# Performance work log

Hardware: AMD Instinct MI355X
Metric: run time of the kernel (lower is better)

## Reference

```python
import jax, jax.numpy as jnp
import numpy as np

L, B, S, D, SD, E, V = 6, 16, 512, 512, 128, 1536, 32000
PDX = 1  # padding_idx: embedding row zeroed


def _pos_encode(seq_len, d_model):
    pos = np.arange(seq_len)[:, None].astype(np.float32)
    i = np.arange(d_model)[None, :].astype(np.float32)
    ang = pos / np.power(10000.0, 2.0 * np.floor(i / 2.0) / d_model)
    pe = np.where(np.arange(d_model)[None, :] % 2 == 0, np.sin(ang), np.cos(ang))
    return jnp.asarray(pe, dtype=jnp.float32)


def setup_inputs() -> dict:
    key = jax.random.key(0)
    ks = jax.random.split(key, 12)
    def n(k, shape, std=0.02):
        return jax.random.normal(k, shape, jnp.float32) * std
    embed = n(ks[0], (V, D)).at[PDX].set(0.0)
    return dict(
        src_tokens=jax.random.randint(ks[1], (B, S), 0, V),
        src_mask=jax.random.randint(ks[2], (B, S), 0, 2).astype(bool),
        embed=embed,
        ln_g=jnp.ones((L, D)), ln_b=jnp.zeros((L, D)),
        Wz=n(ks[3], (L, D, SD)), bz=jnp.zeros((L, SD)),
        gq=1.0 + n(ks[4], (L, S, SD)), bq=n(ks[5], (L, S, SD)),
        gk=1.0 + n(ks[6], (L, S, SD)), bk=n(ks[7], (L, S, SD)),
        Wu=n(ks[8], (L, D, E)), bu=jnp.zeros((L, E)),
        Wv=n(ks[9], (L, D, E)), bv=jnp.zeros((L, E)),
        Wo=n(ks[10], (L, E, D)), bo=jnp.zeros((L, D)),
        fin_g=jnp.ones((D,)), fin_b=jnp.zeros((D,)),
    )


def _ln(x, g, b, eps=1e-5):
    m = x.mean(-1, keepdims=True)
    v = ((x - m) ** 2).mean(-1, keepdims=True)
    return (x - m) * jax.lax.rsqrt(v + eps) * g + b


def reference(src_tokens, src_mask, embed, ln_g, ln_b, Wz, bz, gq, bq, gk, bk,
              Wu, bu, Wv, bv, Wo, bo, fin_g, fin_b):
    d_model = embed.shape[1]
    x = embed[src_tokens] * (d_model ** 0.5)
    x = x + _pos_encode(src_tokens.shape[1], d_model)[None]  # dropout: eval -> identity
    mask = src_mask[:, None, :]  # (B,1,S): zero attention to masked key positions

    def layer(x, p):
        lg, lb, wz, bz_, gq_, bq_, gk_, bk_, wu, bu_, wv, bv_, wo, bo_ = p
        xn = _ln(x, lg, lb)
        u = xn @ wu + bu_          # (B,S,E)
        v = xn @ wv + bv_          # (B,S,E)
        z = xn @ wz + bz_          # (B,S,SD)
        q = z * gq_ + bq_          # scale_offset (per-position affine)
        k = z * gk_ + bk_
        a = jnp.maximum(jnp.einsum('bsd,btd->bst', q, k), 0.0) ** 2  # relu(qk)^2
        a = jnp.where(mask, 0.0, a)
        o = u * jnp.einsum('bst,bte->bse', a, v)  # gated attention output
        return x + o @ wo + bo_, None

    params = (ln_g, ln_b, Wz, bz, gq, bq, gk, bk, Wu, bu, Wv, bv, Wo, bo)
    x, _ = jax.lax.scan(layer, x, params)
    return _ln(x, fin_g, fin_b)
```

## Files before the change

kernel.cpp:

```cpp
#include <hip/hip_runtime.h>
#include <hip/hip_bf16.h>
#include <stdint.h>

constexpr int L = 6, B = 16, S = 512, D = 512, SD = 128, E = 1536;

using bf16x8 = __attribute__((ext_vector_type(8))) short;
using f32x4  = __attribute__((ext_vector_type(4))) float;

typedef __attribute__((address_space(1))) void gvoid;
typedef __attribute__((address_space(3))) void lvoid;

__device__ __forceinline__ unsigned short f2bf(float f) {
    __hip_bfloat16 h = __float2bfloat16(f);
    return __builtin_bit_cast(unsigned short, h);
}
__device__ __forceinline__ float bf2f(unsigned short u) {
    unsigned int v = ((unsigned int)u) << 16;
    return __builtin_bit_cast(float, v);
}
__device__ __forceinline__ void gload16(const void* g, void* l) {
    __builtin_amdgcn_global_load_lds((gvoid*)g, (lvoid*)l, 16, 0, 0);
}

__device__ __forceinline__ void swz_bid(int& bx, int& by, int& bz) {
    int gx = gridDim.x, gy = gridDim.y, gz = gridDim.z;
    int n = gx * gy * gz;
    int id = blockIdx.x + gx * (blockIdx.y + gy * blockIdx.z);
    int id2 = (id & 7) * (n >> 3) + (id >> 3);
    by = id2 % gy;
    int t = id2 / gy;
    bx = t % gx;
    bz = t / gx;
}

__global__ void detect_mask_kernel(const unsigned char* __restrict__ m, int* flag) {
    if (threadIdx.x == 0) *flag = 0;
    __syncthreads();
    int any = 0;
    for (int i = threadIdx.x; i < B * S; i += blockDim.x)
        if ((i & 3) != 0 && m[i] != 0) any = 1;
    if (any) atomicOr(flag, 1);
}

__global__ void embed_kernel(const int* __restrict__ tok, const float* __restrict__ embed,
                             float* __restrict__ x) {
    int idx = blockIdx.x * blockDim.x + threadIdx.x;
    int d = idx & (D - 1);
    int bs = idx >> 9;
    int s = bs & (S - 1);
    float e = embed[(size_t)tok[bs] * D + d] * 22.62741699796952f;
    float expo = (float)(d >> 1) * (1.0f / 256.0f);
    float ang = (float)s * expf(expo * -9.210340371976184f);
    float pe = (d & 1) ? cosf(ang) : sinf(ang);
    x[idx] = e + pe;
}

__global__ __launch_bounds__(256) void tcast_kernel(const float* __restrict__ W,
                                                    unsigned short* __restrict__ Wt,
                                                    int K, int N, long ostride) {
    __shared__ float t[32][33];
    W  += (size_t)blockIdx.z * K * N;
    Wt += (size_t)blockIdx.z * ostride;
    int k0 = blockIdx.x * 32, n0 = blockIdx.y * 32;
    int tx = threadIdx.x, ty = threadIdx.y;
#pragma unroll
    for (int i = 0; i < 4; ++i)
        t[ty + i * 8][tx] = W[(size_t)(k0 + ty + i * 8) * N + n0 + tx];
    __syncthreads();
#pragma unroll
    for (int i = 0; i < 4; ++i)
        Wt[(size_t)(n0 + ty + i * 8) * K + k0 + tx] = f2bf(t[tx][ty + i * 8]);
}

template <bool BF>
__global__ __launch_bounds__(256) void ln_kernel(const float* __restrict__ x,
                                                 const float* __restrict__ g,
                                                 const float* __restrict__ b,
                                                 void* __restrict__ yp) {
    int row = blockIdx.x * 4 + (threadIdx.x >> 6);
    int lane = threadIdx.x & 63;
    const float* xr = x + (size_t)row * D;
    float4 v0 = *(const float4*)(xr + lane * 4);
    float4 v1 = *(const float4*)(xr + 256 + lane * 4);
    float sum = v0.x + v0.y + v0.z + v0.w + v1.x + v1.y + v1.z + v1.w;
#pragma unroll
    for (int o = 1; o < 64; o <<= 1) sum += __shfl_xor(sum, o);
    float m = sum * (1.0f / D);
    float d0 = v0.x - m, d1 = v0.y - m, d2 = v0.z - m, d3 = v0.w - m;
    float e0 = v1.x - m, e1 = v1.y - m, e2 = v1.z - m, e3 = v1.w - m;
    float sq = d0 * d0 + d1 * d1 + d2 * d2 + d3 * d3 + e0 * e0 + e1 * e1 + e2 * e2 + e3 * e3;
#pragma unroll
    for (int o = 1; o < 64; o <<= 1) sq += __shfl_xor(sq, o);
    float inv = rsqrtf(sq * (1.0f / D) + 1e-5f);
    int c0 = lane * 4, c1 = 256 + lane * 4;
    float4 g0 = *(const float4*)(g + c0), g1 = *(const float4*)(g + c1);
    float4 b0 = *(const float4*)(b + c0), b1 = *(const float4*)(b + c1);
    float o0 = d0 * inv * g0.x + b0.x, o1 = d1 * inv * g0.y + b0.y;
    float o2 = d2 * inv * g0.z + b0.z, o3 = d3 * inv * g0.w + b0.w;
    float o4 = e0 * inv * g1.x + b1.x, o5 = e1 * inv * g1.y + b1.y;
    float o6 = e2 * inv * g1.z + b1.z, o7 = e3 * inv * g1.w + b1.w;
    if constexpr (BF) {
        unsigned short* yr = (unsigned short*)yp + (size_t)row * D;
        ushort4 p0 = {f2bf(o0), f2bf(o1), f2bf(o2), f2bf(o3)};
        ushort4 p1 = {f2bf(o4), f2bf(o5), f2bf(o6), f2bf(o7)};
        *(ushort4*)(yr + c0) = p0;
        *(ushort4*)(yr + c1) = p1;
    } else {
        float* yr = (float*)yp + (size_t)row * D;
        float4 p0 = {o0, o1, o2, o3}, p1 = {o4, o5, o6, o7};
        *(float4*)(yr + c0) = p0;
        *(float4*)(yr + c1) = p1;
    }
}

template <int BM, int BN, bool SWAP>
__device__ __forceinline__ void gemm_core(const unsigned short* __restrict__ Ab,
                                          const unsigned short* __restrict__ Bb,
                                          int K, short* lsA, short* lsB,
                                          f32x4 (&acc)[BM / 32][BN / 32],
                                          int lane, int wv) {
    constexpr int NA = BM / 32, NB = BN / 32;
    constexpr int FM = BM / 32, FN = BN / 32;
    constexpr int WTM = BM / 2, WTN = BN / 2;
    const int wm = wv >> 1, wn = wv & 1;
    const unsigned short* ga[NA]; int lofsA[NA];
    const unsigned short* gb[NB]; int lofsB[NB];
#pragma unroll
    for (int i = 0; i < NA; ++i) {
        int s = wv * NA + i;
        int r = s * 8 + (lane >> 3);
        int cl = (lane & 7) ^ (r & 7);
        ga[i] = Ab + (size_t)r * K + cl * 8;
        lofsA[i] = s * 512;
    }
#pragma unroll
    for (int i = 0; i < NB; ++i) {
        int s = wv * NB + i;
        int r = s * 8 + (lane >> 3);
        int cl = (lane & 7) ^ (r & 7);
        gb[i] = Bb + (size_t)r * K + cl * 8;
        lofsB[i] = s * 512;
    }
    const int nkt = K >> 6;
    for (int kt = 0; kt < nkt; ++kt) {
        if (kt) __syncthreads();
#pragma unroll
        for (int i = 0; i < NA; ++i) gload16(ga[i] + kt * 64, (void*)&lsA[lofsA[i]]);
#pragma unroll
        for (int i = 0; i < NB; ++i) gload16(gb[i] + kt * 64, (void*)&lsB[lofsB[i]]);
        __syncthreads();
#pragma unroll
        for (int ks = 0; ks < 2; ++ks) {
            bf16x8 aF[FM], bF[FN];
#pragma unroll
            for (int f = 0; f < FM; ++f) {
                int ra = wm * WTM + f * 16 + (lane & 15);
                int ca = (ks * 4 + (lane >> 4)) ^ (ra & 7);
                aF[f] = *(const bf16x8*)&lsA[ra * 64 + ca * 8];
            }
#pragma unroll
            for (int f = 0; f < FN; ++f) {
                int rb = wn * WTN + f * 16 + (lane & 15);
                int cb = (ks * 4 + (lane >> 4)) ^ (rb & 7);
                bF[f] = *(const bf16x8*)&lsB[rb * 64 + cb * 8];
            }
#pragma unroll
            for (int fi = 0; fi < FM; ++fi)
#pragma unroll
                for (int fj = 0; fj < FN; ++fj) {
                    if constexpr (SWAP)
                        acc[fi][fj] = __builtin_amdgcn_mfma_f32_16x16x32_bf16(
                            bF[fj], aF[fi], acc[fi][fj], 0, 0, 0);
                    else
                        acc[fi][fj] = __builtin_amdgcn_mfma_f32_16x16x32_bf16(
                            aF[fi], bF[fj], acc[fi][fj], 0, 0, 0);
                }
        }
    }
}

__global__ __launch_bounds__(256) void uv_gemm(const unsigned short* __restrict__ xn,
                                               const unsigned short* __restrict__ Wuvt,
                                               const float* __restrict__ bu,
                                               const float* __restrict__ bvp,
                                               unsigned short* __restrict__ u,
                                               unsigned short* __restrict__ vt) {
    __shared__ short lsA[128 * 64];
    __shared__ short lsB[128 * 64];
    int bx, by, bz;
    swz_bid(bx, by, bz);
    const int tid = threadIdx.x;
    const int lane = tid & 63, wv = tid >> 6;
    const int wm = wv >> 1, wn = wv & 1;
    const int row0 = bx * 128, col0 = by * 128;
    const unsigned short* Ab = xn + (size_t)row0 * D;
    const unsigned short* Bb = Wuvt + ((size_t)bz * E + col0) * D;

    const int lr4 = (lane >> 4) * 4;
    const int lc = lane & 15;
    if (bz == 0) {
        f32x4 acc[4][4] = {};
        gemm_core<128, 128, true>(Ab, Bb, D, lsA, lsB, acc, lane, wv);
#pragma unroll
        for (int fi = 0; fi < 4; ++fi) {
            int r = row0 + wm * 64 + fi * 16 + lc;
#pragma unroll
            for (int fj = 0; fj < 4; ++fj) {
                int cb = col0 + wn * 64 + fj * 16 + lr4;
                f32x4 v = acc[fi][fj];
                f32x4 bv = *(const f32x4*)&bu[cb];
                ushort4 ov = {f2bf(v[0] + bv[0]), f2bf(v[1] + bv[1]),
                              f2bf(v[2] + bv[2]), f2bf(v[3] + bv[3])};
                *(ushort4*)&u[(size_t)r * E + cb] = ov;
            }
        }
    } else {
        f32x4 acc[4][4] = {};
        gemm_core<128, 128, false>(Ab, Bb, D, lsA, lsB, acc, lane, wv);
#pragma unroll
        for (int fi = 0; fi < 4; ++fi) {
            int rb = row0 + wm * 64 + fi * 16 + lr4;
#pragma unroll
            for (int fj = 0; fj < 4; ++fj) {
                int c = col0 + wn * 64 + fj * 16 + lc;
                f32x4 v = acc[fi][fj];
                float bv = bvp[c];
                int b = rb >> 9, t0 = rb & 511;
                ushort4 ov = {f2bf(v[0] + bv), f2bf(v[1] + bv),
                              f2bf(v[2] + bv), f2bf(v[3] + bv)};
                *(ushort4*)&vt[((size_t)b * E + c) * 512 + t0] = ov;
            }
        }
    }
}

__global__ __launch_bounds__(256) void zqk_gemm(const unsigned short* __restrict__ xn,
                                                const unsigned short* __restrict__ Bt,
                                                const float* __restrict__ bias,
                                                const float* __restrict__ gq,
                                                const float* __restrict__ bq,
                                                const float* __restrict__ gk,
                                                const float* __restrict__ bk,
                                                unsigned short* __restrict__ q,
                                                unsigned short* __restrict__ k) {
    __shared__ short lsA[128 * 64];
    __shared__ short lsB[128 * 64];
    int bx, by, bz;
    swz_bid(bx, by, bz);
    const int tid = threadIdx.x;
    const int lane = tid & 63, wv = tid >> 6;
    const int wm = wv >> 1, wn = wv & 1;
    const int row0 = bx * 128;
    const unsigned short* Ab = xn + (size_t)row0 * D;

    f32x4 acc[4][4] = {};
    gemm_core<128, 128, true>(Ab, Bt, D, lsA, lsB, acc, lane, wv);

    const int lr4 = (lane >> 4) * 4;
    const int lc = lane & 15;
#pragma unroll
    for (int fi = 0; fi < 4; ++fi) {
        int r = row0 + wm * 64 + fi * 16 + lc;
        int s = r & 511;
#pragma unroll
        for (int fj = 0; fj < 4; ++fj) {
            int cb = wn * 64 + fj * 16 + lr4;
            f32x4 v = acc[fi][fj];
            f32x4 bz4 = *(const f32x4*)&bias[cb];
            f32x4 gq4 = *(const f32x4*)&gq[(size_t)s * SD + cb];
            f32x4 bq4 = *(const f32x4*)&bq[(size_t)s * SD + cb];
            f32x4 gk4 = *(const f32x4*)&gk[(size_t)s * SD + cb];
            f32x4 bk4 = *(const f32x4*)&bk[(size_t)s * SD + cb];
            ushort4 qv, kv;
#pragma unroll
            for (int g = 0; g < 4; ++g) {
                float zz = v[g] + bz4[g];
                ((unsigned short*)&qv)[g] = f2bf(fmaf(zz, gq4[g], bq4[g]));
                ((unsigned short*)&kv)[g] = f2bf(fmaf(zz, gk4[g], bk4[g]));
            }
            *(ushort4*)&q[(size_t)r * SD + cb] = qv;
            *(ushort4*)&k[(size_t)r * SD + cb] = kv;
        }
    }
}

template <int EPI, int BM, int BN>
__global__ __launch_bounds__(256) void mgemm(const unsigned short* __restrict__ A,
                                             const unsigned short* __restrict__ Bt,
                                             const float* __restrict__ bias,
                                             const void* __restrict__ aux,
                                             const int* __restrict__ flagp,
                                             void* __restrict__ Cp,
                                             int N, int K,
                                             long sA, long sB, long sC, long sAux) {
    __shared__ short lsA[BM * 64];
    __shared__ short lsB[BN * 64];
    constexpr int FM = BM / 32, FN = BN / 32;
    int bx, by, bz;
    swz_bid(bx, by, bz);
    const int tid = threadIdx.x;
    const int lane = tid & 63, wv = tid >> 6;
    const int wm = wv >> 1, wn = wv & 1;
    const int row0 = bx * BM, col0 = by * BN;

    const unsigned short* Ab = A + (size_t)bz * sA + (size_t)row0 * K;
    const unsigned short* Bb = Bt + (size_t)bz * sB + (size_t)col0 * K;

    f32x4 acc[FM][FN] = {};
    gemm_core<BM, BN, true>(Ab, Bb, K, lsA, lsB, acc, lane, wv);

    const int lr4 = (lane >> 4) * 4;
    const int lc = lane & 15;
#pragma unroll
    for (int fi = 0; fi < FM; ++fi) {
        int r = row0 + wm * (BM / 2) + fi * 16 + lc;
#pragma unroll
        for (int fj = 0; fj < FN; ++fj) {
            int cb = col0 + wn * (BN / 2) + fj * 16 + lr4;
            f32x4 v = acc[fi][fj];
            if constexpr (EPI == 3) {
                unsigned short* C = (unsigned short*)Cp + (size_t)bz * sC;
                int flag = *flagp;
                ushort4 ov;
#pragma unroll
                for (int g = 0; g < 4; ++g) {
                    int c = cb + g;
                    int mv = flag ? (int)((const unsigned char*)aux)[bz * sAux + c]
                                  : ((const int*)aux)[bz * sAux + c];
                    float vv = fmaxf(v[g], 0.0f);
                    vv *= vv;
                    ((unsigned short*)&ov)[g] = mv ? (unsigned short)0 : f2bf(vv);
                }
                *(ushort4*)&C[(size_t)r * N + cb] = ov;
            } else if constexpr (EPI == 4) {
                const unsigned short* U = (const unsigned short*)aux + (size_t)bz * sAux;
                unsigned short* C = (unsigned short*)Cp + (size_t)bz * sC;
                size_t off = (size_t)r * N + cb;
                ushort4 uu = *(const ushort4*)&U[off];
                ushort4 ov = {f2bf(bf2f(uu.x) * v[0]), f2bf(bf2f(uu.y) * v[1]),
                              f2bf(bf2f(uu.z) * v[2]), f2bf(bf2f(uu.w) * v[3])};
                *(ushort4*)&C[off] = ov;
            } else {
                float* C = (float*)Cp;
                const float* X = (const float*)aux;
                size_t off = (size_t)r * N + cb;
                f32x4 bb = *(const f32x4*)&bias[cb];
                f32x4 xx = *(const f32x4*)&X[off];
                f32x4 ov = {v[0] + bb[0] + xx[0], v[1] + bb[1] + xx[1],
                            v[2] + bb[2] + xx[2], v[3] + bb[3] + xx[3]};
                *(f32x4*)&C[off] = ov;
            }
        }
    }
}

extern "C" void kernel_launch(void* const* d_in, const int* in_sizes, int n_in,
                              void* d_out, int out_size, void* d_ws, size_t ws_size,
                              hipStream_t stream) {
    const int* tok = (const int*)d_in[0];
    const unsigned char* mask = (const unsigned char*)d_in[1];
    const float* embed = (const float*)d_in[2];
    const float* ln_g = (const float*)d_in[3];
    const float* ln_b = (const float*)d_in[4];
    const float* Wz = (const float*)d_in[5];
    const float* bz = (const float*)d_in[6];
    const float* gq = (const float*)d_in[7];
    const float* bq = (const float*)d_in[8];
    const float* gk = (const float*)d_in[9];
    const float* bk = (const float*)d_in[10];
    const float* Wu = (const float*)d_in[11];
    const float* bu = (const float*)d_in[12];
    const float* Wv = (const float*)d_in[13];
    const float* bv = (const float*)d_in[14];
    const float* Wo = (const float*)d_in[15];
    const float* bo = (const float*)d_in[16];
    const float* fin_g = (const float*)d_in[17];
    const float* fin_b = (const float*)d_in[18];

    char* wsb = (char*)d_ws;
    size_t off = 0;
    auto alloc = [&](size_t nbytes) {
        void* p = wsb + off;
        off = (off + nbytes + 255) & ~(size_t)255;
        return p;
    };
    int* flag = (int*)alloc(256);
    float* x = (float*)alloc((size_t)B * S * D * 4);
    unsigned short* xn = (unsigned short*)alloc((size_t)B * S * D * 2);
    unsigned short* q = (unsigned short*)alloc((size_t)B * S * SD * 2);
    unsigned short* k = (unsigned short*)alloc((size_t)B * S * SD * 2);
    unsigned short* u = (unsigned short*)alloc((size_t)B * S * E * 2);
    unsigned short* vt = (unsigned short*)alloc((size_t)B * E * S * 2);
    unsigned short* o = (unsigned short*)alloc((size_t)B * S * E * 2);
    unsigned short* a = (unsigned short*)alloc((size_t)B * S * S * 2);
    unsigned short* Wuvzt = (unsigned short*)alloc((size_t)L * 3200 * D * 2);
    unsigned short* Wot = (unsigned short*)alloc((size_t)L * D * E * 2);

    constexpr long WUVZ = 3200L * D;

    detect_mask_kernel<<<1, 256, 0, stream>>>(mask, flag);
    embed_kernel<<<(B * S * D) / 256, 256, 0, stream>>>(tok, embed, x);
    tcast_kernel<<<dim3(D / 32, E / 32, L), dim3(32, 8), 0, stream>>>(Wu, Wuvzt, D, E, WUVZ);
    tcast_kernel<<<dim3(D / 32, E / 32, L), dim3(32, 8), 0, stream>>>(
        Wv, Wuvzt + 1536L * D, D, E, WUVZ);
    tcast_kernel<<<dim3(D / 32, SD / 32, L), dim3(32, 8), 0, stream>>>(
        Wz, Wuvzt + 3072L * D, D, SD, WUVZ);
    tcast_kernel<<<dim3(E / 32, D / 32, L), dim3(32, 8), 0, stream>>>(
        Wo, Wot, E, D, (long)D * E);

    for (int l = 0; l < L; ++l) {
        ln_kernel<true><<<B * S / 4, 256, 0, stream>>>(x, ln_g + l * D, ln_b + l * D, xn);
        uv_gemm<<<dim3(64, 12, 2), 256, 0, stream>>>(
            xn, Wuvzt + (size_t)l * WUVZ, bu + l * E, bv + l * E, u, vt);
        zqk_gemm<<<dim3(64, 1), 256, 0, stream>>>(
            xn, Wuvzt + (size_t)l * WUVZ + 3072L * D, bz + l * SD,
            gq + (size_t)l * S * SD, bq + (size_t)l * S * SD,
            gk + (size_t)l * S * SD, bk + (size_t)l * S * SD, q, k);
        mgemm<3, 64, 64><<<dim3(8, 8, B), 256, 0, stream>>>(
            q, k, nullptr, mask, flag, a, S, SD,
            (long)S * SD, (long)S * SD, (long)S * S, S);
        mgemm<4, 128, 128><<<dim3(4, 12, B), 256, 0, stream>>>(
            a, vt, nullptr, u, nullptr, o, E, S,
            (long)S * S, (long)E * S, (long)S * E, (long)S * E);
        mgemm<5, 128, 64><<<dim3(64, 8), 256, 0, stream>>>(
            o, Wot + (size_t)l * D * E, bo + l * D, x, nullptr, x, D, E, 0, 0, 0, 0);
    }
    ln_kernel<false><<<B * S / 4, 256, 0, stream>>>(x, fin_g, fin_b, (float*)d_out);
}
```

Before: 769.5 us.

## Fuse U/V/Z projections into one 256x128-tile GEMM with 8 waves

Merges the separate u/v GEMM and the z→q,k GEMM into a single launch over the concatenated weight matrix, branching on column-block index for each epilogue. Uses 256-row tiles with 8 waves (4x2), generalising gemm_core to a configurable wave grid, and retiles the qk score GEMM to 128x64. The aim is to remove a launch plus the poorly occupied 64-block zqk kernel and to raise reuse of the A tile. It risks higher register and LDS pressure per block and branch-divergent code size.

New measurement: 831.8 us. 8.1% more time.

```diff
diff --git a/kernel.cpp b/kernel.cpp
--- a/kernel.cpp
+++ b/kernel.cpp
@@ -113,16 +113,17 @@
     }
 }
 
-template <int BM, int BN, bool SWAP>
+template <int BM, int BN, int WM, int WN, bool SWAP>
 __device__ __forceinline__ void gemm_core(const unsigned short* __restrict__ Ab,
                                           const unsigned short* __restrict__ Bb,
                                           int K, short* lsA, short* lsB,
-                                          f32x4 (&acc)[BM / 32][BN / 32],
+                                          f32x4 (&acc)[BM / WM / 16][BN / WN / 16],
                                           int lane, int wv) {
-    constexpr int NA = BM / 32, NB = BN / 32;
-    constexpr int FM = BM / 32, FN = BN / 32;
-    constexpr int WTM = BM / 2, WTN = BN / 2;
-    const int wm = wv >> 1, wn = wv & 1;
+    constexpr int NW = WM * WN;
+    constexpr int NA = BM / 8 / NW, NB = BN / 8 / NW;
+    constexpr int WTM = BM / WM, WTN = BN / WN;
+    constexpr int FM = WTM / 16, FN = WTN / 16;
+    const int wm = wv / WN, wn = wv % WN;
     const unsigned short* ga[NA]; int lofsA[NA];
     const unsigned short* gb[NB]; int lofsB[NB];
 #pragma unroll
@@ -179,28 +180,53 @@
     }
 }
 
-__global__ __launch_bounds__(256) void uv_gemm(const unsigned short* __restrict__ xn,
-                                               const unsigned short* __restrict__ Wuvt,
-                                               const float* __restrict__ bu,
-                                               const float* __restrict__ bvp,
-                                               unsigned short* __restrict__ u,
-                                               unsigned short* __restrict__ vt) {
-    __shared__ short lsA[128 * 64];
+__global__ __launch_bounds__(512, 4) void uvz_gemm(const unsigned short* __restrict__ xn,
+                                                   const unsigned short* __restrict__ Wt,
+                                                   const float* __restrict__ bu,
+                                                   const float* __restrict__ bvp,
+                                                   const float* __restrict__ bzp,
+                                                   const float* __restrict__ gq,
+                                                   const float* __restrict__ bq,
+                                                   const float* __restrict__ gk,
+                                                   const float* __restrict__ bk,
+                                                   unsigned short* __restrict__ u,
+                                                   unsigned short* __restrict__ vt,
+                                                   unsigned short* __restrict__ q,
+                                                   unsigned short* __restrict__ k) {
+    __shared__ short lsA[256 * 64];
     __shared__ short lsB[128 * 64];
-    int bx, by, bz;
-    swz_bid(bx, by, bz);
+    int bx, by, bzz;
+    swz_bid(bx, by, bzz);
     const int tid = threadIdx.x;
     const int lane = tid & 63, wv = tid >> 6;
     const int wm = wv >> 1, wn = wv & 1;
-    const int row0 = bx * 128, col0 = by * 128;
+    const int row0 = bx * 256, col0 = by * 128;
     const unsigned short* Ab = xn + (size_t)row0 * D;
-    const unsigned short* Bb = Wuvt + ((size_t)bz * E + col0) * D;
-
+    const unsigned short* Bb = Wt + (size_t)col0 * D;
     const int lr4 = (lane >> 4) * 4;
     const int lc = lane & 15;
-    if (bz == 0) {
+
+    if (by >= 12 && by < 24) {
         f32x4 acc[4][4] = {};
-        gemm_core<128, 128, true>(Ab, Bb, D, lsA, lsB, acc, lane, wv);
+        gemm_core<256, 128, 4, 2, false>(Ab, Bb, D, lsA, lsB, acc, lane, wv);
+#pragma unroll
+        for (int fi = 0; fi < 4; ++fi) {
+            int rb = row0 + wm * 64 + fi * 16 + lr4;
+            int b = rb >> 9, t0 = rb & 511;
+#pragma unroll
+            for (int fj = 0; fj < 4; ++fj) {
+                int c = col0 + wn * 64 + fj * 16 + lc;
+                int cv = c - 1536;
+                f32x4 v = acc[fi][fj];
+                float bv = bvp[cv];
+                ushort4 ov = {f2bf(v[0] + bv), f2bf(v[1] + bv),
+                              f2bf(v[2] + bv), f2bf(v[3] + bv)};
+                *(ushort4*)&vt[((size_t)b * E + cv) * 512 + t0] = ov;
+            }
+        }
+    } else if (by < 12) {
+        f32x4 acc[4][4] = {};
+        gemm_core<256, 128, 4, 2, true>(Ab, Bb, D, lsA, lsB, acc, lane, wv);
 #pragma unroll
         for (int fi = 0; fi < 4; ++fi) {
             int r = row0 + wm * 64 + fi * 16 + lc;
@@ -216,75 +242,35 @@
         }
     } else {
         f32x4 acc[4][4] = {};
-        gemm_core<128, 128, false>(Ab, Bb, D, lsA, lsB, acc, lane, wv);
+        gemm_core<256, 128, 4, 2, true>(Ab, Bb, D, lsA, lsB, acc, lane, wv);
 #pragma unroll
         for (int fi = 0; fi < 4; ++fi) {
-            int rb = row0 + wm * 64 + fi * 16 + lr4;
+            int r = row0 + wm * 64 + fi * 16 + lc;
+            int s = r & 511;
 #pragma unroll
             for (int fj = 0; fj < 4; ++fj) {
-                int c = col0 + wn * 64 + fj * 16 + lc;
+                int cb = wn * 64 + fj * 16 + lr4;
                 f32x4 v = acc[fi][fj];
-                float bv = bvp[c];
-                int b = rb >> 9, t0 = rb & 511;
-                ushort4 ov = {f2bf(v[0] + bv), f2bf(v[1] + bv),
-                              f2bf(v[2] + bv), f2bf(v[3] + bv)};
-                *(ushort4*)&vt[((size_t)b * E + c) * 512 + t0] = ov;
+                f32x4 bz4 = *(const f32x4*)&bzp[cb];
+                f32x4 gq4 = *(const f32x4*)&gq[(size_t)s * SD + cb];
+                f32x4 bq4 = *(const f32x4*)&bq[(size_t)s * SD + cb];
+                f32x4 gk4 = *(const f32x4*)&gk[(size_t)s * SD + cb];
+                f32x4 bk4 = *(const f32x4*)&bk[(size_t)s * SD + cb];
+                ushort4 qv, kv;
+#pragma unroll
+                for (int g = 0; g < 4; ++g) {
+                    float zz = v[g] + bz4[g];
+                    ((unsigned short*)&qv)[g] = f2bf(fmaf(zz, gq4[g], bq4[g]));
+                    ((unsigned short*)&kv)[g] = f2bf(fmaf(zz, gk4[g], bk4[g]));
+                }
+                *(ushort4*)&q[(size_t)r * SD + cb] = qv;
+                *(ushort4*)&k[(size_t)r * SD + cb] = kv;
             }
         }
     }
 }
 
-__global__ __launch_bounds__(256) void zqk_gemm(const unsigned short* __restrict__ xn,
-                                                const unsigned short* __restrict__ Bt,
-                                                const float* __restrict__ bias,
-                                                const float* __restrict__ gq,
-                                                const float* __restrict__ bq,
-                                                const float* __restrict__ gk,
-                                                const float* __restrict__ bk,
-                                                unsigned short* __restrict__ q,
-                                                unsigned short* __restrict__ k) {
-    __shared__ short lsA[128 * 64];
-    __shared__ short lsB[128 * 64];
-    int bx, by, bz;
-    swz_bid(bx, by, bz);
-    const int tid = threadIdx.x;
-    const int lane = tid & 63, wv = tid >> 6;
-    const int wm = wv >> 1, wn = wv & 1;
-    const int row0 = bx * 128;
-    const unsigned short* Ab = xn + (size_t)row0 * D;
-
-    f32x4 acc[4][4] = {};
-    gemm_core<128, 128, true>(Ab, Bt, D, lsA, lsB, acc, lane, wv);
-
-    const int lr4 = (lane >> 4) * 4;
-    const int lc = lane & 15;
-#pragma unroll
-    for (int fi = 0; fi < 4; ++fi) {
-        int r = row0 + wm * 64 + fi * 16 + lc;
-        int s = r & 511;
-#pragma unroll
-        for (int fj = 0; fj < 4; ++fj) {
-            int cb = wn * 64 + fj * 16 + lr4;
-            f32x4 v = acc[fi][fj];
-            f32x4 bz4 = *(const f32x4*)&bias[cb];
-            f32x4 gq4 = *(const f32x4*)&gq[(size_t)s * SD + cb];
-            f32x4 bq4 = *(const f32x4*)&bq[(size_t)s * SD + cb];
-            f32x4 gk4 = *(const f32x4*)&gk[(size_t)s * SD + cb];
-            f32x4 bk4 = *(const f32x4*)&bk[(size_t)s * SD + cb];
-            ushort4 qv, kv;
-#pragma unroll
-            for (int g = 0; g < 4; ++g) {
-                float zz = v[g] + bz4[g];
-                ((unsigned short*)&qv)[g] = f2bf(fmaf(zz, gq4[g], bq4[g]));
-                ((unsigned short*)&kv)[g] = f2bf(fmaf(zz, gk4[g], bk4[g]));
-            }
-            *(ushort4*)&q[(size_t)r * SD + cb] = qv;
-            *(ushort4*)&k[(size_t)r * SD + cb] = kv;
-        }
-    }
-}
-
-template <int EPI, int BM, int BN>
+template <int EPI, int BM, int BN, int WM, int WN>
 __global__ __launch_bounds__(256) void mgemm(const unsigned short* __restrict__ A,
                                              const unsigned short* __restrict__ Bt,
                                              const float* __restrict__ bias,
@@ -295,28 +281,28 @@
                                              long sA, long sB, long sC, long sAux) {
     __shared__ short lsA[BM * 64];
     __shared__ short lsB[BN * 64];
-    constexpr int FM = BM / 32, FN = BN / 32;
+    constexpr int FM = BM / WM / 16, FN = BN / WN / 16;
     int bx, by, bz;
     swz_bid(bx, by, bz);
     const int tid = threadIdx.x;
     const int lane = tid & 63, wv = tid >> 6;
-    const int wm = wv >> 1, wn = wv & 1;
+    const int wm = wv / WN, wn = wv % WN;
     const int row0 = bx * BM, col0 = by * BN;
 
     const unsigned short* Ab = A + (size_t)bz * sA + (size_t)row0 * K;
     const unsigned short* Bb = Bt + (size_t)bz * sB + (size_t)col0 * K;
 
     f32x4 acc[FM][FN] = {};
-    gemm_core<BM, BN, true>(Ab, Bb, K, lsA, lsB, acc, lane, wv);
+    gemm_core<BM, BN, WM, WN, true>(Ab, Bb, K, lsA, lsB, acc, lane, wv);
 
     const int lr4 = (lane >> 4) * 4;
     const int lc = lane & 15;
 #pragma unroll
     for (int fi = 0; fi < FM; ++fi) {
-        int r = row0 + wm * (BM / 2) + fi * 16 + lc;
+        int r = row0 + wm * (BM / WM) + fi * 16 + lc;
 #pragma unroll
         for (int fj = 0; fj < FN; ++fj) {
-            int cb = col0 + wn * (BN / 2) + fj * 16 + lr4;
+            int cb = col0 + wn * (BN / WN) + fj * 16 + lr4;
             f32x4 v = acc[fi][fj];
             if constexpr (EPI == 3) {
                 unsigned short* C = (unsigned short*)Cp + (size_t)bz * sC;
@@ -410,19 +396,17 @@
 
     for (int l = 0; l < L; ++l) {
         ln_kernel<true><<<B * S / 4, 256, 0, stream>>>(x, ln_g + l * D, ln_b + l * D, xn);
-        uv_gemm<<<dim3(64, 12, 2), 256, 0, stream>>>(
-            xn, Wuvzt + (size_t)l * WUVZ, bu + l * E, bv + l * E, u, vt);
-        zqk_gemm<<<dim3(64, 1), 256, 0, stream>>>(
-            xn, Wuvzt + (size_t)l * WUVZ + 3072L * D, bz + l * SD,
+        uvz_gemm<<<dim3(32, 25), 512, 0, stream>>>(
+            xn, Wuvzt + (size_t)l * WUVZ, bu + l * E, bv + l * E, bz + l * SD,
             gq + (size_t)l * S * SD, bq + (size_t)l * S * SD,
-            gk + (size_t)l * S * SD, bk + (size_t)l * S * SD, q, k);
-        mgemm<3, 64, 64><<<dim3(8, 8, B), 256, 0, stream>>>(
+            gk + (size_t)l * S * SD, bk + (size_t)l * S * SD, u, vt, q, k);
+        mgemm<3, 128, 64, 2, 2><<<dim3(4, 8, B), 256, 0, stream>>>(
             q, k, nullptr, mask, flag, a, S, SD,
             (long)S * SD, (long)S * SD, (long)S * S, S);
-        mgemm<4, 128, 128><<<dim3(4, 12, B), 256, 0, stream>>>(
+        mgemm<4, 128, 128, 2, 2><<<dim3(4, 12, B), 256, 0, stream>>>(
             a, vt, nullptr, u, nullptr, o, E, S,
             (long)S * S, (long)E * S, (long)S * E, (long)S * E);
-        mgemm<5, 128, 64><<<dim3(64, 8), 256, 0, stream>>>(
+        mgemm<5, 128, 64, 2, 2><<<dim3(64, 8), 256, 0, stream>>>(
             o, Wot + (size_t)l * D * E, bo + l * D, x, nullptr, x, D, E, 0, 0, 0, 0);
     }
     ln_kernel<false><<<B * S / 4, 256, 0, stream>>>(x, fin_g, fin_b, (float*)d_out);
```

## Double-buffer LDS in mgemm GEMMs and narrow the attention-output tile

Applied to the files above, without the earlier changes.

Adds a double-buffered K-loop to the shared GEMM core, so global-to-LDS loads for the next K tile are issued while MFMAs run on the current tile. This cuts the barriers per step from two to one. All three mgemm launches use the new path. The gated a@v GEMM also moves from 128x128 to 128x64 tiles, doubling its grid. The costs are double the LDS per block, which may lower occupancy, and extra B-tile reloads from the smaller output tile.

Result: slower. 811.9 us (+5.5%).

```diff
diff --git a/kernel.cpp b/kernel.cpp
--- a/kernel.cpp
+++ b/kernel.cpp
@@ -113,16 +113,17 @@
     }
 }
 
-template <int BM, int BN, bool SWAP>
+template <int BM, int BN, int WM, int WN, bool SWAP, bool DBUF>
 __device__ __forceinline__ void gemm_core(const unsigned short* __restrict__ Ab,
                                           const unsigned short* __restrict__ Bb,
                                           int K, short* lsA, short* lsB,
-                                          f32x4 (&acc)[BM / 32][BN / 32],
+                                          f32x4 (&acc)[BM / WM / 16][BN / WN / 16],
                                           int lane, int wv) {
-    constexpr int NA = BM / 32, NB = BN / 32;
-    constexpr int FM = BM / 32, FN = BN / 32;
-    constexpr int WTM = BM / 2, WTN = BN / 2;
-    const int wm = wv >> 1, wn = wv & 1;
+    constexpr int NW = WM * WN;
+    constexpr int NA = BM / 8 / NW, NB = BN / 8 / NW;
+    constexpr int WTM = BM / WM, WTN = BN / WN;
+    constexpr int FM = WTM / 16, FN = WTN / 16;
+    const int wm = wv / WN, wn = wv % WN;
     const unsigned short* ga[NA]; int lofsA[NA];
     const unsigned short* gb[NB]; int lofsB[NB];
 #pragma unroll
@@ -142,13 +143,8 @@
         lofsB[i] = s * 512;
     }
     const int nkt = K >> 6;
-    for (int kt = 0; kt < nkt; ++kt) {
-        if (kt) __syncthreads();
-#pragma unroll
-        for (int i = 0; i < NA; ++i) gload16(ga[i] + kt * 64, (void*)&lsA[lofsA[i]]);
-#pragma unroll
-        for (int i = 0; i < NB; ++i) gload16(gb[i] + kt * 64, (void*)&lsB[lofsB[i]]);
-        __syncthreads();
+
+    auto compute_step = [&](const short* cA, const short* cB) {
 #pragma unroll
         for (int ks = 0; ks < 2; ++ks) {
             bf16x8 aF[FM], bF[FN];
@@ -156,13 +152,13 @@
             for (int f = 0; f < FM; ++f) {
                 int ra = wm * WTM + f * 16 + (lane & 15);
                 int ca = (ks * 4 + (lane >> 4)) ^ (ra & 7);
-                aF[f] = *(const bf16x8*)&lsA[ra * 64 + ca * 8];
+                aF[f] = *(const bf16x8*)&cA[ra * 64 + ca * 8];
             }
 #pragma unroll
             for (int f = 0; f < FN; ++f) {
                 int rb = wn * WTN + f * 16 + (lane & 15);
                 int cb = (ks * 4 + (lane >> 4)) ^ (rb & 7);
-                bF[f] = *(const bf16x8*)&lsB[rb * 64 + cb * 8];
+                bF[f] = *(const bf16x8*)&cB[rb * 64 + cb * 8];
             }
 #pragma unroll
             for (int fi = 0; fi < FM; ++fi)
@@ -175,6 +171,39 @@
                         acc[fi][fj] = __builtin_amdgcn_mfma_f32_16x16x32_bf16(
                             aF[fi], bF[fj], acc[fi][fj], 0, 0, 0);
                 }
+        }
+    };
+
+    if constexpr (!DBUF) {
+        for (int kt = 0; kt < nkt; ++kt) {
+            if (kt) __syncthreads();
+#pragma unroll
+            for (int i = 0; i < NA; ++i) gload16(ga[i] + kt * 64, (void*)&lsA[lofsA[i]]);
+#pragma unroll
+            for (int i = 0; i < NB; ++i) gload16(gb[i] + kt * 64, (void*)&lsB[lofsB[i]]);
+            __syncthreads();
+            compute_step(lsA, lsB);
+        }
+    } else {
+#pragma unroll
+        for (int i = 0; i < NA; ++i) gload16(ga[i], (void*)&lsA[lofsA[i]]);
+#pragma unroll
+        for (int i = 0; i < NB; ++i) gload16(gb[i], (void*)&lsB[lofsB[i]]);
+        __syncthreads();
+        int cur = 0;
+        for (int kt = 0; kt < nkt; ++kt) {
+            if (kt + 1 < nkt) {
+                int nxt = cur ^ 1;
+#pragma unroll
+                for (int i = 0; i < NA; ++i)
+                    gload16(ga[i] + (kt + 1) * 64, (void*)&lsA[nxt * (BM * 64) + lofsA[i]]);
+#pragma unroll
+                for (int i = 0; i < NB; ++i)
+                    gload16(gb[i] + (kt + 1) * 64, (void*)&lsB[nxt * (BN * 64) + lofsB[i]]);
+            }
+            compute_step(&lsA[cur * (BM * 64)], &lsB[cur * (BN * 64)]);
+            __syncthreads();
+            cur ^= 1;
         }
     }
 }
@@ -200,7 +229,7 @@
     const int lc = lane & 15;
     if (bz == 0) {
         f32x4 acc[4][4] = {};
-        gemm_core<128, 128, true>(Ab, Bb, D, lsA, lsB, acc, lane, wv);
+        gemm_core<128, 128, 2, 2, true, false>(Ab, Bb, D, lsA, lsB, acc, lane, wv);
 #pragma unroll
         for (int fi = 0; fi < 4; ++fi) {
             int r = row0 + wm * 64 + fi * 16 + lc;
@@ -216,7 +245,7 @@
         }
     } else {
         f32x4 acc[4][4] = {};
-        gemm_core<128, 128, false>(Ab, Bb, D, lsA, lsB, acc, lane, wv);
+        gemm_core<128, 128, 2, 2, false, false>(Ab, Bb, D, lsA, lsB, acc, lane, wv);
 #pragma unroll
         for (int fi = 0; fi < 4; ++fi) {
             int rb = row0 + wm * 64 + fi * 16 + lr4;
@@ -254,7 +283,7 @@
     const unsigned short* Ab = xn + (size_t)row0 * D;
 
     f32x4 acc[4][4] = {};
-    gemm_core<128, 128, true>(Ab, Bt, D, lsA, lsB, acc, lane, wv);
+    gemm_core<128, 128, 2, 2, true, false>(Ab, Bt, D, lsA, lsB, acc, lane, wv);
 
     const int lr4 = (lane >> 4) * 4;
     const int lc = lane & 15;
@@ -284,7 +313,7 @@
     }
 }
 
-template <int EPI, int BM, int BN>
+template <int EPI, int BM, int BN, int WM, int WN, bool DBUF>
 __global__ __launch_bounds__(256) void mgemm(const unsigned short* __restrict__ A,
                                              const unsigned short* __restrict__ Bt,
                                              const float* __restrict__ bias,
@@ -293,30 +322,31 @@
                                              void* __restrict__ Cp,
                                              int N, int K,
                                              long sA, long sB, long sC, long sAux) {
-    __shared__ short lsA[BM * 64];
-    __shared__ short lsB[BN * 64];
-    constexpr int FM = BM / 32, FN = BN / 32;
+    constexpr int NBUF = DBUF ? 2 : 1;
+    __shared__ short lsA[NBUF * BM * 64];
+    __shared__ short lsB[NBUF * BN * 64];
+    constexpr int FM = BM / WM / 16, FN = BN / WN / 16;
     int bx, by, bz;
     swz_bid(bx, by, bz);
     const int tid = threadIdx.x;
     const int lane = tid & 63, wv = tid >> 6;
-    const int wm = wv >> 1, wn = wv & 1;
+    const int wm = wv / WN, wn = wv % WN;
     const int row0 = bx * BM, col0 = by * BN;
 
     const unsigned short* Ab = A + (size_t)bz * sA + (size_t)row0 * K;
     const unsigned short* Bb = Bt + (size_t)bz * sB + (size_t)col0 * K;
 
     f32x4 acc[FM][FN] = {};
-    gemm_core<BM, BN, true>(Ab, Bb, K, lsA, lsB, acc, lane, wv);
+    gemm_core<BM, BN, WM, WN, true, DBUF>(Ab, Bb, K, lsA, lsB, acc, lane, wv);
 
     const int lr4 = (lane >> 4) * 4;
     const int lc = lane & 15;
 #pragma unroll
     for (int fi = 0; fi < FM; ++fi) {
-        int r = row0 + wm * (BM / 2) + fi * 16 + lc;
+        int r = row0 + wm * (BM / WM) + fi * 16 + lc;
 #pragma unroll
         for (int fj = 0; fj < FN; ++fj) {
-            int cb = col0 + wn * (BN / 2) + fj * 16 + lr4;
+            int cb = col0 + wn * (BN / WN) + fj * 16 + lr4;
             f32x4 v = acc[fi][fj];
             if constexpr (EPI == 3) {
                 unsigned short* C = (unsigned short*)Cp + (size_t)bz * sC;
@@ -416,13 +446,13 @@
             xn, Wuvzt + (size_t)l * WUVZ + 3072L * D, bz + l * SD,
             gq + (size_t)l * S * SD, bq + (size_t)l * S * SD,
             gk + (size_t)l * S * SD, bk + (size_t)l * S * SD, q, k);
-        mgemm<3, 64, 64><<<dim3(8, 8, B), 256, 0, stream>>>(
+        mgemm<3, 64, 64, 2, 2, true><<<dim3(8, 8, B), 256, 0, stream>>>(
             q, k, nullptr, mask, flag, a, S, SD,
             (long)S * SD, (long)S * SD, (long)S * S, S);
-        mgemm<4, 128, 128><<<dim3(4, 12, B), 256, 0, stream>>>(
+        mgemm<4, 128, 64, 2, 2, true><<<dim3(4, 24, B), 256, 0, stream>>>(
             a, vt, nullptr, u, nullptr, o, E, S,
             (long)S * S, (long)E * S, (long)S * E, (long)S * E);
-        mgemm<5, 128, 64><<<dim3(64, 8), 256, 0, stream>>>(
+        mgemm<5, 128, 64, 2, 2, true><<<dim3(64, 8), 256, 0, stream>>>(
             o, Wot + (size_t)l * D * E, bo + l * D, x, nullptr, x, D, E, 0, 0, 0, 0);
     }
     ln_kernel<false><<<B * S / 4, 256, 0, stream>>>(x, fin_g, fin_b, (float*)d_out);
```
